# Optimization experiments

Measured on AMD Instinct MI355X. Metric: run time of the kernel, lower is better.

Reference implementation:

```python
import jax, jax.numpy as jnp
import numpy as np

H = 64          # HIDDEN_DIM
V = 64          # VOCAB_SIZE
LN_EPS = 1e-5   # torch LayerNorm default
D_EPS = 1e-6    # denom epsilon in delta rule
MEM_SCALE = 1.0 # forward default arg


def setup_inputs() -> dict:
    key = jax.random.key(0)
    ks = jax.random.split(key, 8)
    B, L = 16, 2048
    s = lambda k, shape: (jax.random.normal(k, shape, jnp.float32) * 0.05)
    return {
        "seq": jax.random.randint(ks[0], (B, L), 0, V),
        "embed": s(ks[1], (V, H)),
        "W1": s(ks[2], (H, 2 * H)), "b1": jnp.zeros((2 * H,), jnp.float32),
        "W2": s(ks[3], (2 * H, H)), "b2": jnp.zeros((H,), jnp.float32),
        "gamma": jnp.ones((H,), jnp.float32), "beta": jnp.zeros((H,), jnp.float32),
        "Wr": s(ks[4], (H, H)), "br": jnp.zeros((H,), jnp.float32),
        "Wo": s(ks[5], (H, V)), "bo": jnp.zeros((V,), jnp.float32),
    }


def reference(seq, embed, W1, b1, W2, b2, gamma, beta, Wr, br, Wo, bo):
    h = embed[seq]                                  # (B, L, H)
    ff = jax.nn.relu(h @ W1 + b1) @ W2 + b2         # (B, L, H)
    x = h + ff
    mu = x.mean(-1, keepdims=True)
    var = x.var(-1, keepdims=True)                  # biased, as torch LayerNorm
    h = (x - mu) / jnp.sqrt(var + LN_EPS) * gamma + beta

    B = h.shape[0]
    keys = jnp.swapaxes(h[:, :-1, :], 0, 1)         # (L-1, B, H): all but last token

    def step(M, k):                                  # M: (B, H, H), k: (B, H)
        v_pred = jnp.einsum('bij,bj->bi', M, k)
        denom = (k * k).sum(-1, keepdims=True) + D_EPS
        dv = k - v_pred / denom
        M = M + MEM_SCALE * dv[:, :, None] * k[:, None, :]
        return M, None

    M0 = jnp.zeros((B, H, H), h.dtype)
    M, _ = jax.lax.scan(step, M0, keys)

    q = h[:, -1, :]                                  # last token as query
    ctx = jnp.einsum('bij,bj->bi', M, q)             # (B, H)
    return (ctx @ Wr + br) @ Wo + bo                 # (B, V)
```

## Files before the change

kernel.cpp:

```cpp
#include <hip/hip_runtime.h>

#define HDIM 64
#define LSEQ 2048
#define BATCH 16
#define LN_EPS 1e-5f
#define D_EPS 1e-6f
#define NSEG 16
#define CPS 8

typedef unsigned short u16;
typedef unsigned int   u32;

__device__ __forceinline__ float bf2f(u16 v) {
    return __uint_as_float(((u32)v) << 16);
}
__device__ __forceinline__ u16 f2bf(float f) {
    u32 u = __float_as_uint(f);
    return (u16)((u + 0x7FFFu + ((u >> 16) & 1u)) >> 16);
}

#define P_SW1   0
#define P_SW2   33792
#define P_ET    68608
#define P_HIDT  86016
#define P_RED1  120832
#define P_RED2  121888
#define P_SMU   122944
#define P_SRSTD 123216
#define H_ROWS  123488
#define H_INVD  158304
#define SMEM_BYTES 158816
#define C_S     0
#define C_V     17408
#define C_BM    34816
#define C_Z     39168
#define C_GM    43520
#define C_IVD   44608

__global__ __launch_bounds__(256, 1) void fused_pc_kernel(
    const int* __restrict__ seq, const float* __restrict__ embed,
    const float* __restrict__ W1, const float* __restrict__ b1,
    const float* __restrict__ W2, const float* __restrict__ b2,
    const float* __restrict__ gamma, const float* __restrict__ beta,
    u32* __restrict__ PK, u16* __restrict__ q_ws)
{
    __shared__ __align__(16) char smem[SMEM_BYTES];
    const int t = threadIdx.x;
    const int b = blockIdx.x >> 4;
    const int s = blockIdx.x & 15;
    const int tok0 = 1920 - 128 * s;

    float* hrows  = (float*)(smem + H_ROWS);
    float* invd_l = (float*)(smem + H_INVD);

    {
        float* sW1   = (float*)(smem + P_SW1);
        float* sW2   = (float*)(smem + P_SW2);
        float* eT    = (float*)(smem + P_ET);
        float* hidT  = (float*)(smem + P_HIDT);
        float* red1  = (float*)(smem + P_RED1);
        float* red2  = (float*)(smem + P_RED2);
        float* smu   = (float*)(smem + P_SMU);
        float* srstd = (float*)(smem + P_SRSTD);

        {
            const float4* s1 = (const float4*)W1;
#pragma unroll
            for (int q = 0; q < 8; ++q) {
                const int m = t + 256 * q;
                const int row = m >> 5, col = m & 31;
                *(float4*)&sW1[row * 132 + col * 4] = s1[m];
            }
            const float4* s2 = (const float4*)W2;
#pragma unroll
            for (int q = 0; q < 8; ++q) {
                const int m = t + 256 * q;
                const int row = m >> 4, col = m & 15;
                *(float4*)&sW2[row * 68 + col * 4] = s2[m];
            }
        }

        for (int it = 0; it < 2; ++it) {
            const int g0 = b * LSEQ + tok0 + 64 * it;
            __syncthreads();

            {
                const int tk = t >> 2, p = t & 3;
                const int v = seq[g0 + tk];
                const float* er = embed + v * HDIM + 16 * p;
#pragma unroll
                for (int q = 0; q < 4; ++q) {
                    const float4 ev = *(const float4*)(er + 4 * q);
                    const int d = 16 * p + 4 * q;
                    eT[(d + 0) * 68 + tk] = ev.x;
                    eT[(d + 1) * 68 + tk] = ev.y;
                    eT[(d + 2) * 68 + tk] = ev.z;
                    eT[(d + 3) * 68 + tk] = ev.w;
                }
            }
            __syncthreads();

            const int r = t >> 4;
            const int c = t & 15;

            {
                float acc0[4][4], acc1[4][4];
#pragma unroll
                for (int o = 0; o < 4; ++o) {
                    const float bA = b1[4 * c + o];
                    const float bB = b1[64 + 4 * c + o];
#pragma unroll
                    for (int j = 0; j < 4; ++j) { acc0[j][o] = bA; acc1[j][o] = bB; }
                }
                for (int k = 0; k < 64; ++k) {
                    const float4 ev = *(const float4*)&eT[k * 68 + 4 * r];
                    const float4 wa = *(const float4*)&sW1[k * 132 + 4 * c];
                    const float4 wb = *(const float4*)&sW1[k * 132 + 64 + 4 * c];
                    const float e4[4] = {ev.x, ev.y, ev.z, ev.w};
                    const float a4[4] = {wa.x, wa.y, wa.z, wa.w};
                    const float b4[4] = {wb.x, wb.y, wb.z, wb.w};
#pragma unroll
                    for (int j = 0; j < 4; ++j)
#pragma unroll
                        for (int o = 0; o < 4; ++o) {
                            acc0[j][o] = fmaf(e4[j], a4[o], acc0[j][o]);
                            acc1[j][o] = fmaf(e4[j], b4[o], acc1[j][o]);
                        }
                }
#pragma unroll
                for (int o = 0; o < 4; ++o)
#pragma unroll
                    for (int j = 0; j < 4; ++j) {
                        hidT[(4 * c + o) * 68 + 4 * r + j]      = fmaxf(acc0[j][o], 0.f);
                        hidT[(64 + 4 * c + o) * 68 + 4 * r + j] = fmaxf(acc1[j][o], 0.f);
                    }
            }
            __syncthreads();

            {
                float acc[4][4];
#pragma unroll
                for (int o = 0; o < 4; ++o) {
                    const float bv = b2[4 * c + o];
#pragma unroll
                    for (int j = 0; j < 4; ++j) acc[j][o] = bv;
                }
                for (int k = 0; k < 128; ++k) {
                    const float4 hv = *(const float4*)&hidT[k * 68 + 4 * r];
                    const float4 wv = *(const float4*)&sW2[k * 68 + 4 * c];
                    const float h4[4] = {hv.x, hv.y, hv.z, hv.w};
                    const float w4[4] = {wv.x, wv.y, wv.z, wv.w};
#pragma unroll
                    for (int j = 0; j < 4; ++j)
#pragma unroll
                        for (int o = 0; o < 4; ++o)
                            acc[j][o] = fmaf(h4[j], w4[o], acc[j][o]);
                }
#pragma unroll
                for (int o = 0; o < 4; ++o)
#pragma unroll
                    for (int j = 0; j < 4; ++j)
                        eT[(4 * c + o) * 68 + (4 * r + j)] += acc[j][o];
            }
            __syncthreads();

            {
                const int tk = t & 63, p = t >> 6;
                float sv = 0.f, q = 0.f;
#pragma unroll
                for (int i = 0; i < 16; ++i) {
                    const float x = eT[(16 * p + i) * 68 + tk];
                    sv += x;
                    q = fmaf(x, x, q);
                }
                red1[p * 66 + tk] = sv;
                red2[p * 66 + tk] = q;
            }
            __syncthreads();
            if (t < 64) {
                const float sv = ((red1[0 * 66 + t] + red1[1 * 66 + t]) + (red1[2 * 66 + t] + red1[3 * 66 + t]));
                const float qq = ((red2[0 * 66 + t] + red2[1 * 66 + t]) + (red2[2 * 66 + t] + red2[3 * 66 + t]));
                const float mu  = sv * (1.0f / 64.0f);
                const float var = qq * (1.0f / 64.0f) - mu * mu;
                smu[t]   = mu;
                srstd[t] = 1.0f / sqrtf(var + LN_EPS);
            }
            __syncthreads();

            {
                const int tk = t >> 2, p = t & 3;
                const float mu = smu[tk], rstd = srstd[tk];
                const int lrow = 64 * it + tk;
                float hh = 0.f;
#pragma unroll
                for (int i2 = 0; i2 < 8; ++i2) {
                    const int d = 16 * p + 2 * i2;
                    const float x0 = eT[(d + 0) * 68 + tk];
                    const float x1 = eT[(d + 1) * 68 + tk];
                    const float o0 = (x0 - mu) * rstd * gamma[d + 0] + beta[d + 0];
                    const float o1 = (x1 - mu) * rstd * gamma[d + 1] + beta[d + 1];
                    const u16 r0 = f2bf(o0), r1 = f2bf(o1);
                    const float q0f = bf2f(r0), q1f = bf2f(r1);
                    hh = fmaf(q0f, q0f, hh);
                    hh = fmaf(q1f, q1f, hh);
                    hrows[lrow * 68 + d]     = q0f;
                    hrows[lrow * 68 + d + 1] = q1f;
                    if (s == 0 && lrow == 127) {
                        q_ws[b * 64 + d]     = r0;
                        q_ws[b * 64 + d + 1] = r1;
                    }
                }
                red1[p * 66 + tk] = hh;
            }
            __syncthreads();
            if (t < 64) {
                const float hh = ((red1[0 * 66 + t] + red1[1 * 66 + t]) + (red1[2 * 66 + t] + red1[3 * 66 + t]));
                invd_l[64 * it + t] = 1.0f / (hh + D_EPS);
            }
        }
    }
    __syncthreads();

    if (s == 0 && t < 64) hrows[127 * 68 + t] = 0.f;

    {
        float* S     = (float*)(smem + C_S);
        float* V     = (float*)(smem + C_V);
        float* Bm    = (float*)(smem + C_BM);
        float* Z     = (float*)(smem + C_Z);
        float* Gm    = (float*)(smem + C_GM);
        float* ivd_s = (float*)(smem + C_IVD);

        for (int idx = t; idx < 64 * 64; idx += 256) {
            const int m = idx >> 6, n = idx & 63;
            S[m * 68 + n] = (m == n) ? 1.0f : 0.0f;
            V[m * 68 + n] = 0.0f;
        }

        for (int cc = 0; cc < CPS; ++cc) {
            const int base = 127 - 16 * cc;
            __syncthreads();

            if (t < 16) ivd_s[t] = invd_l[base - t];
            __syncthreads();

            {
                const int i = t >> 4, j = t & 15;
                if (i > j) {
                    const float* ra = &hrows[(base - i) * 68];
                    const float* rb = &hrows[(base - j) * 68];
                    float acc = 0.f;
#pragma unroll
                    for (int m = 0; m < 64; m += 4) {
                        const float4 a  = *(const float4*)&ra[m];
                        const float4 bb = *(const float4*)&rb[m];
                        acc += a.x * bb.x + a.y * bb.y + a.z * bb.z + a.w * bb.w;
                    }
                    Gm[i * 17 + j] = acc * ivd_s[j];
                }
            }
            __syncthreads();

            if (t < 64) {
                const int n = t;
                float Breg[16];
#pragma unroll
                for (int i = 0; i < 16; ++i) {
                    float acc = hrows[(base - i) * 68 + n];
#pragma unroll
                    for (int j = 0; j < 16; ++j)
                        if (j < i) acc = fmaf(-Gm[i * 17 + j], Breg[j], acc);
                    Breg[i] = acc;
                    Bm[i * 68 + n] = acc;
                }
            }
            __syncthreads();

            {
                const int i  = t & 15;
                const int n0 = (t >> 4) * 4;
                float4 z = make_float4(0.f, 0.f, 0.f, 0.f);
#pragma unroll
                for (int mq = 0; mq < 16; ++mq) {
                    const float4 bq = *(const float4*)&Bm[i * 68 + mq * 4];
                    const float4 s0 = *(const float4*)&S[(mq * 4 + 0) * 68 + n0];
                    const float4 s1 = *(const float4*)&S[(mq * 4 + 1) * 68 + n0];
                    const float4 s2 = *(const float4*)&S[(mq * 4 + 2) * 68 + n0];
                    const float4 s3 = *(const float4*)&S[(mq * 4 + 3) * 68 + n0];
                    z.x = fmaf(bq.x, s0.x, fmaf(bq.y, s1.x, fmaf(bq.z, s2.x, fmaf(bq.w, s3.x, z.x))));
                    z.y = fmaf(bq.x, s0.y, fmaf(bq.y, s1.y, fmaf(bq.z, s2.y, fmaf(bq.w, s3.y, z.y))));
                    z.z = fmaf(bq.x, s0.z, fmaf(bq.y, s1.z, fmaf(bq.z, s2.z, fmaf(bq.w, s3.z, z.z))));
                    z.w = fmaf(bq.x, s0.w, fmaf(bq.y, s1.w, fmaf(bq.z, s2.w, fmaf(bq.w, s3.w, z.w))));
                }
                *(float4*)&Z[i * 68 + n0] = z;
            }
            __syncthreads();

            {
                const int n0 = (t & 15) * 4;
                const int mh = t >> 4;
                float iv16[16];
#pragma unroll
                for (int q4 = 0; q4 < 4; ++q4) {
                    const float4 v4 = *(const float4*)&ivd_s[4 * q4];
                    iv16[4*q4+0] = v4.x; iv16[4*q4+1] = v4.y;
                    iv16[4*q4+2] = v4.z; iv16[4*q4+3] = v4.w;
                }
                float4 sacc[4], vacc[4];
#pragma unroll
                for (int p = 0; p < 4; ++p) {
                    sacc[p] = *(float4*)&S[(mh + 16 * p) * 68 + n0];
                    vacc[p] = *(float4*)&V[(mh + 16 * p) * 68 + n0];
                }
#pragma unroll
                for (int j = 0; j < 16; ++j) {
                    const float4 zq = *(const float4*)&Z[j * 68 + n0];
                    const float iv = iv16[j];
                    float4 ztq;
                    ztq.x = zq.x * iv; ztq.y = zq.y * iv;
                    ztq.z = zq.z * iv; ztq.w = zq.w * iv;
                    const float* kr = &hrows[(base - j) * 68];
                    const float k0 = kr[mh];
                    const float k1 = kr[mh + 16];
                    const float k2 = kr[mh + 32];
                    const float k3 = kr[mh + 48];
                    vacc[0].x = fmaf(k0, zq.x, vacc[0].x); vacc[0].y = fmaf(k0, zq.y, vacc[0].y);
                    vacc[0].z = fmaf(k0, zq.z, vacc[0].z); vacc[0].w = fmaf(k0, zq.w, vacc[0].w);
                    vacc[1].x = fmaf(k1, zq.x, vacc[1].x); vacc[1].y = fmaf(k1, zq.y, vacc[1].y);
                    vacc[1].z = fmaf(k1, zq.z, vacc[1].z); vacc[1].w = fmaf(k1, zq.w, vacc[1].w);
                    vacc[2].x = fmaf(k2, zq.x, vacc[2].x); vacc[2].y = fmaf(k2, zq.y, vacc[2].y);
                    vacc[2].z = fmaf(k2, zq.z, vacc[2].z); vacc[2].w = fmaf(k2, zq.w, vacc[2].w);
                    vacc[3].x = fmaf(k3, zq.x, vacc[3].x); vacc[3].y = fmaf(k3, zq.y, vacc[3].y);
                    vacc[3].z = fmaf(k3, zq.z, vacc[3].z); vacc[3].w = fmaf(k3, zq.w, vacc[3].w);
                    sacc[0].x = fmaf(-k0, ztq.x, sacc[0].x); sacc[0].y = fmaf(-k0, ztq.y, sacc[0].y);
                    sacc[0].z = fmaf(-k0, ztq.z, sacc[0].z); sacc[0].w = fmaf(-k0, ztq.w, sacc[0].w);
                    sacc[1].x = fmaf(-k1, ztq.x, sacc[1].x); sacc[1].y = fmaf(-k1, ztq.y, sacc[1].y);
                    sacc[1].z = fmaf(-k1, ztq.z, sacc[1].z); sacc[1].w = fmaf(-k1, ztq.w, sacc[1].w);
                    sacc[2].x = fmaf(-k2, ztq.x, sacc[2].x); sacc[2].y = fmaf(-k2, ztq.y, sacc[2].y);
                    sacc[2].z = fmaf(-k2, ztq.z, sacc[2].z); sacc[2].w = fmaf(-k2, ztq.w, sacc[2].w);
                    sacc[3].x = fmaf(-k3, ztq.x, sacc[3].x); sacc[3].y = fmaf(-k3, ztq.y, sacc[3].y);
                    sacc[3].z = fmaf(-k3, ztq.z, sacc[3].z); sacc[3].w = fmaf(-k3, ztq.w, sacc[3].w);
                }
#pragma unroll
                for (int p = 0; p < 4; ++p) {
                    *(float4*)&S[(mh + 16 * p) * 68 + n0] = sacc[p];
                    *(float4*)&V[(mh + 16 * p) * 68 + n0] = vacc[p];
                }
            }
        }
        __syncthreads();

        u32* pk = PK + ((size_t)(b * NSEG + s) << 12);
        for (int idx = t; idx < 4096; idx += 256) {
            const int j = idx >> 6, i = idx & 63;
            const u32 sb = ((u32)f2bf(S[i * 68 + j])) << 16;
            const u32 vb = (u32)f2bf(V[i * 68 + j]);
            pk[idx] = sb | vb;
        }
    }
}

__global__ __launch_bounds__(256, 1) void final_kernel(
    const u16* __restrict__ q_ws, const u32* __restrict__ PK,
    const float* __restrict__ Wr, const float* __restrict__ br,
    const float* __restrict__ Wo, const float* __restrict__ bo,
    float* __restrict__ out)
{
    const int b    = blockIdx.x;
    const int t    = threadIdx.x;
    const int lane = t & 63;
    const int p    = t >> 6;

    __shared__ float psum[4][72];
    __shared__ float rl[64];
    __shared__ float cs[64], rs[64];

    rl[lane] = bf2f(q_ws[b * 64 + lane]);

    float ctxp = 0.f;
    u32 cur[16], nxt[16];
    {
        const u32* pk0 = PK + ((size_t)(b * NSEG + 0) << 12);
#pragma unroll
        for (int jj = 0; jj < 16; ++jj)
            cur[jj] = pk0[(p * 16 + jj) * 64 + lane];
    }
    __syncthreads();

    for (int s = 0; s < NSEG; ++s) {
        const int sn = (s + 1 < NSEG) ? s + 1 : s;
        const u32* pkn = PK + ((size_t)(b * NSEG + sn) << 12);
#pragma unroll
        for (int jj = 0; jj < 16; ++jj)
            nxt[jj] = pkn[(p * 16 + jj) * 64 + lane];

        float accr = 0.f;
#pragma unroll
        for (int jj = 0; jj < 16; ++jj) {
            const u32 pv = cur[jj];
            const float Sv = __uint_as_float(pv & 0xFFFF0000u);
            const float Vv = __uint_as_float(pv << 16);
            const float rj = rl[p * 16 + jj];
            accr = fmaf(Sv, rj, accr);
            ctxp = fmaf(Vv, rj, ctxp);
        }
        psum[p][lane] = accr;
        __syncthreads();
        const float rn = (psum[0][lane] + psum[1][lane]) + (psum[2][lane] + psum[3][lane]);
        __syncthreads();
        rl[lane] = rn;

#pragma unroll
        for (int jj = 0; jj < 16; ++jj) cur[jj] = nxt[jj];
    }

    psum[p][lane] = ctxp;
    __syncthreads();
    if (t < 64)
        cs[t] = (psum[0][t] + psum[1][t]) + (psum[2][t] + psum[3][t]);
    __syncthreads();

    float rv = (p == 0) ? br[lane] : 0.f;
#pragma unroll
    for (int i = 0; i < 16; ++i)
        rv = fmaf(cs[p * 16 + i], Wr[(p * 16 + i) * HDIM + lane], rv);
    psum[p][lane] = rv;
    __syncthreads();
    if (t < 64)
        rs[t] = (psum[0][t] + psum[1][t]) + (psum[2][t] + psum[3][t]);
    __syncthreads();

    float ov = (p == 0) ? bo[lane] : 0.f;
#pragma unroll
    for (int i = 0; i < 16; ++i)
        ov = fmaf(rs[p * 16 + i], Wo[(p * 16 + i) * HDIM + lane], ov);
    psum[p][lane] = ov;
    __syncthreads();
    if (t < 64)
        out[(size_t)b * HDIM + t] = (psum[0][t] + psum[1][t]) + (psum[2][t] + psum[3][t]);
}

extern "C" void kernel_launch(void* const* d_in, const int* in_sizes, int n_in,
                              void* d_out, int out_size, void* d_ws, size_t ws_size,
                              hipStream_t stream)
{
    const int*   seq   = (const int*)  d_in[0];
    const float* embed = (const float*)d_in[1];
    const float* W1    = (const float*)d_in[2];
    const float* b1    = (const float*)d_in[3];
    const float* W2    = (const float*)d_in[4];
    const float* b2    = (const float*)d_in[5];
    const float* gamma = (const float*)d_in[6];
    const float* beta  = (const float*)d_in[7];
    const float* Wr    = (const float*)d_in[8];
    const float* br    = (const float*)d_in[9];
    const float* Wo    = (const float*)d_in[10];
    const float* bo    = (const float*)d_in[11];

    u32* pk_ws = (u32*)d_ws;
    u16* q_ws  = (u16*)(pk_ws + (size_t)BATCH * NSEG * 4096);
    float* outp = (float*)d_out;

    hipLaunchKernelGGL(fused_pc_kernel, dim3(BATCH * NSEG), dim3(256), 0, stream,
                       seq, embed, W1, b1, W2, b2, gamma, beta, pk_ws, q_ws);
    hipLaunchKernelGGL(final_kernel, dim3(BATCH), dim3(256), 0, stream,
                       q_ws, pk_ws, Wr, br, Wo, bo, outp);
}
```

Measured before the change: 139.3 us.

## Fuse final reduction into main kernel via global atomic counter barrier

Merges the two kernels into one. Every block bumps a global counter after writing its packed segment, and the first 16 blocks spin until all 256 blocks are done before running the segment-chaining reduction and output projection. This removes a kernel launch and its inter-kernel gap, but adds a memset, a spin-wait, and depends on all 256 blocks being co-resident (one per CU) to avoid deadlock.

```diff
diff --git a/kernel.cpp b/kernel.cpp
--- a/kernel.cpp
+++ b/kernel.cpp
@@ -36,13 +36,20 @@
 #define C_Z     39168
 #define C_GM    43520
 #define C_IVD   44608
-
-__global__ __launch_bounds__(256, 1) void fused_pc_kernel(
+#define F_PSUM  0
+#define F_RL    1152
+#define F_CS    1408
+#define F_RS    1664
+
+__global__ __launch_bounds__(256, 1) void fused_kernel(
     const int* __restrict__ seq, const float* __restrict__ embed,
     const float* __restrict__ W1, const float* __restrict__ b1,
     const float* __restrict__ W2, const float* __restrict__ b2,
     const float* __restrict__ gamma, const float* __restrict__ beta,
-    u32* __restrict__ PK, u16* __restrict__ q_ws)
+    const float* __restrict__ Wr, const float* __restrict__ br,
+    const float* __restrict__ Wo, const float* __restrict__ bo,
+    u32* __restrict__ PK, u16* __restrict__ q_ws,
+    u32* __restrict__ counter, float* __restrict__ out)
 {
     __shared__ __align__(16) char smem[SMEM_BYTES];
     const int t = threadIdx.x;
@@ -358,86 +365,97 @@
             pk[idx] = sb | vb;
         }
     }
-}
-
-__global__ __launch_bounds__(256, 1) void final_kernel(
-    const u16* __restrict__ q_ws, const u32* __restrict__ PK,
-    const float* __restrict__ Wr, const float* __restrict__ br,
-    const float* __restrict__ Wo, const float* __restrict__ bo,
-    float* __restrict__ out)
-{
-    const int b    = blockIdx.x;
-    const int t    = threadIdx.x;
-    const int lane = t & 63;
-    const int p    = t >> 6;
-
-    __shared__ float psum[4][72];
-    __shared__ float rl[64];
-    __shared__ float cs[64], rs[64];
-
-    rl[lane] = bf2f(q_ws[b * 64 + lane]);
-
-    float ctxp = 0.f;
-    u32 cur[16], nxt[16];
+
+    __threadfence();
+    __syncthreads();
+    if (t == 0) atomicAdd(counter, 1u);
+
+    if (blockIdx.x >= BATCH) return;
+
     {
-        const u32* pk0 = PK + ((size_t)(b * NSEG + 0) << 12);
-#pragma unroll
-        for (int jj = 0; jj < 16; ++jj)
-            cur[jj] = pk0[(p * 16 + jj) * 64 + lane];
+        if (t == 0) {
+            while (__hip_atomic_load(counter, __ATOMIC_ACQUIRE,
+                                     __HIP_MEMORY_SCOPE_AGENT) < 256u) {
+                __builtin_amdgcn_s_sleep(8);
+            }
+        }
+        __syncthreads();
+        __threadfence();
+
+        float* psum = (float*)(smem + F_PSUM);
+        float* rl   = (float*)(smem + F_RL);
+        float* cs   = (float*)(smem + F_CS);
+        float* rs   = (float*)(smem + F_RS);
+
+        const int fb   = blockIdx.x;
+        const int lane = t & 63;
+        const int p    = t >> 6;
+
+        rl[lane] = bf2f(q_ws[fb * 64 + lane]);
+
+        float ctxp = 0.f;
+        u32 cur[16], nxt[16];
+        {
+            const u32* pk0 = PK + ((size_t)(fb * NSEG + 0) << 12);
+#pragma unroll
+            for (int jj = 0; jj < 16; ++jj)
+                cur[jj] = pk0[(p * 16 + jj) * 64 + lane];
+        }
+        __syncthreads();
+
+        for (int ss = 0; ss < NSEG; ++ss) {
+            const int sn = (ss + 1 < NSEG) ? ss + 1 : ss;
+            const u32* pkn = PK + ((size_t)(fb * NSEG + sn) << 12);
+#pragma unroll
+            for (int jj = 0; jj < 16; ++jj)
+                nxt[jj] = pkn[(p * 16 + jj) * 64 + lane];
+
+            float accr = 0.f;
+#pragma unroll
+            for (int jj = 0; jj < 16; ++jj) {
+                const u32 pv = cur[jj];
+                const float Sv = __uint_as_float(pv & 0xFFFF0000u);
+                const float Vv = __uint_as_float(pv << 16);
+                const float rj = rl[p * 16 + jj];
+                accr = fmaf(Sv, rj, accr);
+                ctxp = fmaf(Vv, rj, ctxp);
+            }
+            psum[p * 72 + lane] = accr;
+            __syncthreads();
+            const float rn = (psum[0 * 72 + lane] + psum[1 * 72 + lane])
+                           + (psum[2 * 72 + lane] + psum[3 * 72 + lane]);
+            __syncthreads();
+            rl[lane] = rn;
+
+#pragma unroll
+            for (int jj = 0; jj < 16; ++jj) cur[jj] = nxt[jj];
+        }
+
+        psum[p * 72 + lane] = ctxp;
+        __syncthreads();
+        if (t < 64)
+            cs[t] = (psum[0 * 72 + t] + psum[1 * 72 + t]) + (psum[2 * 72 + t] + psum[3 * 72 + t]);
+        __syncthreads();
+
+        float rv = (p == 0) ? br[lane] : 0.f;
+#pragma unroll
+        for (int i = 0; i < 16; ++i)
+            rv = fmaf(cs[p * 16 + i], Wr[(p * 16 + i) * HDIM + lane], rv);
+        psum[p * 72 + lane] = rv;
+        __syncthreads();
+        if (t < 64)
+            rs[t] = (psum[0 * 72 + t] + psum[1 * 72 + t]) + (psum[2 * 72 + t] + psum[3 * 72 + t]);
+        __syncthreads();
+
+        float ov = (p == 0) ? bo[lane] : 0.f;
+#pragma unroll
+        for (int i = 0; i < 16; ++i)
+            ov = fmaf(rs[p * 16 + i], Wo[(p * 16 + i) * HDIM + lane], ov);
+        psum[p * 72 + lane] = ov;
+        __syncthreads();
+        if (t < 64)
+            out[(size_t)fb * HDIM + t] = (psum[0 * 72 + t] + psum[1 * 72 + t]) + (psum[2 * 72 + t] + psum[3 * 72 + t]);
     }
-    __syncthreads();
-
-    for (int s = 0; s < NSEG; ++s) {
-        const int sn = (s + 1 < NSEG) ? s + 1 : s;
-        const u32* pkn = PK + ((size_t)(b * NSEG + sn) << 12);
-#pragma unroll
-        for (int jj = 0; jj < 16; ++jj)
-            nxt[jj] = pkn[(p * 16 + jj) * 64 + lane];
-
-        float accr = 0.f;
-#pragma unroll
-        for (int jj = 0; jj < 16; ++jj) {
-            const u32 pv = cur[jj];
-            const float Sv = __uint_as_float(pv & 0xFFFF0000u);
-            const float Vv = __uint_as_float(pv << 16);
-            const float rj = rl[p * 16 + jj];
-            accr = fmaf(Sv, rj, accr);
-            ctxp = fmaf(Vv, rj, ctxp);
-        }
-        psum[p][lane] = accr;
-        __syncthreads();
-        const float rn = (psum[0][lane] + psum[1][lane]) + (psum[2][lane] + psum[3][lane]);
-        __syncthreads();
-        rl[lane] = rn;
-
-#pragma unroll
-        for (int jj = 0; jj < 16; ++jj) cur[jj] = nxt[jj];
-    }
-
-    psum[p][lane] = ctxp;
-    __syncthreads();
-    if (t < 64)
-        cs[t] = (psum[0][t] + psum[1][t]) + (psum[2][t] + psum[3][t]);
-    __syncthreads();
-
-    float rv = (p == 0) ? br[lane] : 0.f;
-#pragma unroll
-    for (int i = 0; i < 16; ++i)
-        rv = fmaf(cs[p * 16 + i], Wr[(p * 16 + i) * HDIM + lane], rv);
-    psum[p][lane] = rv;
-    __syncthreads();
-    if (t < 64)
-        rs[t] = (psum[0][t] + psum[1][t]) + (psum[2][t] + psum[3][t]);
-    __syncthreads();
-
-    float ov = (p == 0) ? bo[lane] : 0.f;
-#pragma unroll
-    for (int i = 0; i < 16; ++i)
-        ov = fmaf(rs[p * 16 + i], Wo[(p * 16 + i) * HDIM + lane], ov);
-    psum[p][lane] = ov;
-    __syncthreads();
-    if (t < 64)
-        out[(size_t)b * HDIM + t] = (psum[0][t] + psum[1][t]) + (psum[2][t] + psum[3][t]);
 }
 
 extern "C" void kernel_launch(void* const* d_in, const int* in_sizes, int n_in,
@@ -457,12 +475,13 @@
     const float* Wo    = (const float*)d_in[10];
     const float* bo    = (const float*)d_in[11];
 
-    u32* pk_ws = (u32*)d_ws;
-    u16* q_ws  = (u16*)(pk_ws + (size_t)BATCH * NSEG * 4096);
-    float* outp = (float*)d_out;
-
-    hipLaunchKernelGGL(fused_pc_kernel, dim3(BATCH * NSEG), dim3(256), 0, stream,
-                       seq, embed, W1, b1, W2, b2, gamma, beta, pk_ws, q_ws);
-    hipLaunchKernelGGL(final_kernel, dim3(BATCH), dim3(256), 0, stream,
-                       q_ws, pk_ws, Wr, br, Wo, bo, outp);
+    u32* pk_ws   = (u32*)d_ws;
+    u16* q_ws    = (u16*)(pk_ws + (size_t)BATCH * NSEG * 4096);
+    u32* counter = (u32*)(q_ws + BATCH * HDIM);
+    float* outp  = (float*)d_out;
+
+    hipMemsetAsync(counter, 0, sizeof(u32), stream);
+    hipLaunchKernelGGL(fused_kernel, dim3(BATCH * NSEG), dim3(256), 0, stream,
+                       seq, embed, W1, b1, W2, b2, gamma, beta,
+                       Wr, br, Wo, bo, pk_ws, q_ws, counter, outp);
 }
```

Result: slower. 166.6 us (+19.6%).
